# Kernel optimization log

Measured on AMD Instinct MI355X. Metric: run time of the kernel, lower is better.

Reference implementation:

```python
import jax, jax.numpy as jnp
import numpy as np

N_NODES = 50000


def gcn_conv(x, src, dst, norm, W, b, n_nodes):
    """One GCNConv layer: out = scatter_add(norm * (x @ W)[src] -> dst) + b.
    src/dst already include self loops; norm is the symmetric D^-1/2 A_hat D^-1/2 edge weight."""
    h = x @ W  # [N, C_out]
    msg = h[src] * norm[:, None]  # [E+N, C_out]
    out = jax.ops.segment_sum(msg, dst, num_segments=n_nodes)
    return out + b


def build_norm(edge_index, n_nodes):
    """Add self loops and compute symmetric GCN normalization (PyG GCNConv default)."""
    loop = jnp.arange(n_nodes, dtype=edge_index.dtype)
    src = jnp.concatenate([edge_index[0], loop])
    dst = jnp.concatenate([edge_index[1], loop])
    deg = jax.ops.segment_sum(jnp.ones_like(dst, dtype=jnp.float32), dst, num_segments=n_nodes)
    dinv = jnp.where(deg > 0, jax.lax.rsqrt(jnp.maximum(deg, 1.0)), 0.0)
    norm = dinv[src] * dinv[dst]
    return src, dst, norm


def setup_inputs() -> dict:
    key = jax.random.key(0)
    ks = jax.random.split(key, 8)
    in_c, h1, h2, out_c = 768, 256, 128, 2
    x = jax.random.normal(ks[0], (N_NODES, in_c), dtype=jnp.float32)
    edge_index = jax.random.randint(ks[1], (2, 800000), 0, N_NODES, dtype=jnp.int32)
    W1 = jax.random.normal(ks[2], (in_c, h1), dtype=jnp.float32) * 0.02
    b1 = jnp.zeros((h1,), dtype=jnp.float32)
    W2 = jax.random.normal(ks[3], (h1, h2), dtype=jnp.float32) * 0.02
    b2 = jnp.zeros((h2,), dtype=jnp.float32)
    W3 = jax.random.normal(ks[4], (h2, out_c), dtype=jnp.float32) * 0.02
    b3 = jnp.zeros((out_c,), dtype=jnp.float32)
    return {"x": x, "edge_index": edge_index, "W1": W1, "b1": b1,
            "W2": W2, "b2": b2, "W3": W3, "b3": b3}


def reference(x, edge_index, W1, b1, W2, b2, W3, b3):
    n = x.shape[0]
    src, dst, norm = build_norm(edge_index, n)
    # Dropout is identity in eval mode (training=False), so it is omitted.
    h = jax.nn.relu(gcn_conv(x, src, dst, norm, W1, b1, n))
    h = jax.nn.relu(gcn_conv(h, src, dst, norm, W2, b2, n))
    h = gcn_conv(h, src, dst, norm, W3, b3, n)
    return jax.nn.sigmoid(h)
```

## Files before the change

### kernel.cpp

```cpp
#include <hip/hip_runtime.h>
#include <math.h>

typedef short s16x8 __attribute__((ext_vector_type(8)));
typedef __bf16 b16x8 __attribute__((ext_vector_type(8)));
typedef float f32x4 __attribute__((ext_vector_type(4)));
typedef float f32x2 __attribute__((ext_vector_type(2)));
typedef unsigned int u32x4 __attribute__((ext_vector_type(4)));

__device__ inline short f2bf(float f) {
    unsigned u = __float_as_uint(f);
    unsigned r = u + 0x7FFFu + ((u >> 16) & 1u);
    return (short)(r >> 16);
}
__device__ inline float bf2f(unsigned short u) {
    return __uint_as_float(((unsigned)u) << 16);
}

#define GLDS16(g, l)                                                            \
    __builtin_amdgcn_global_load_lds(                                           \
        (const __attribute__((address_space(1))) void*)(g),                     \
        (__attribute__((address_space(3))) void*)(l), 16, 0, 0)


__device__ inline void make_wt_elem(const float* __restrict__ W, short* __restrict__ Wt,
                                    int K, int N, int idx) {
    int NB = N >> 7;
    int j = idx & 7;
    int l = (idx >> 3) & 63;
    int nt = (idx >> 9) & 7;
    int rest = idx >> 12;
    int b = rest % NB;
    int c = rest / NB;
    int k = c * 32 + (l >> 4) * 8 + j;
    int n = b * 128 + nt * 16 + (l & 15);
    Wt[idx] = f2bf(W[(size_t)k * N + n]);
}

__global__ void prep_kernel(const int* __restrict__ dst, int* __restrict__ cnt, int E,
                            const float* __restrict__ W1, short* __restrict__ Wt1,
                            const float* __restrict__ W2, short* __restrict__ Wt2,
                            int cb, int w1b) {
    int b = blockIdx.x;
    int tid = threadIdx.x;
    if (b < cb) {
        int e = b * 256 + tid;
        if (e < E) atomicAdd(&cnt[dst[e]], 1);
    } else if (b < cb + w1b) {
        int idx = (b - cb) * 256 + tid;
        make_wt_elem(W1, Wt1, 768, 256, idx);
    } else {
        int idx = (b - cb - w1b) * 256 + tid;
        make_wt_elem(W2, Wt2, 256, 128, idx);
    }
}


__global__ __launch_bounds__(1024) void blockscan_kernel(const int* __restrict__ cnt,
                                                         int* __restrict__ rp,
                                                         int* __restrict__ bsum, int n) {
    __shared__ int sdata[1024];
    int tid = threadIdx.x;
    int i = blockIdx.x * 1024 + tid;
    int v = (i < n) ? cnt[i] : 0;
    sdata[tid] = v;
    __syncthreads();
    for (int off = 1; off < 1024; off <<= 1) {
        int t = 0;
        if (tid >= off) t = sdata[tid - off];
        __syncthreads();
        sdata[tid] += t;
        __syncthreads();
    }
    if (i < n) rp[i] = sdata[tid] - v;
    if (tid == 1023) bsum[blockIdx.x] = sdata[1023];
}

__global__ void topscan_kernel(int* bsum, int nb) {
    int lane = threadIdx.x;
    int carry = 0;
    for (int base = 0; base < nb; base += 64) {
        int idx = base + lane;
        int orig = (idx < nb) ? bsum[idx] : 0;
        int v = orig;
        for (int off = 1; off < 64; off <<= 1) {
            int t = __shfl_up(v, off, 64);
            if (lane >= off) v += t;
        }
        if (idx < nb) bsum[idx] = carry + v - orig;
        carry += __shfl(v, 63, 64);
    }
}

__global__ __launch_bounds__(1024) void fixup_kernel(int* __restrict__ rp,
                                                     const int* __restrict__ bsum,
                                                     const int* __restrict__ cnt,
                                                     int* __restrict__ cursor,
                                                     float* __restrict__ dinv,
                                                     int n, int E) {
    int i = blockIdx.x * 1024 + threadIdx.x;
    if (i < n) {
        int r = rp[i] + bsum[blockIdx.x];
        rp[i] = r;
        cursor[i] = r;
        dinv[i] = rsqrtf((float)cnt[i] + 1.0f);
    }
    if (i == 0) rp[n] = E;
}

__global__ void fill_kernel(const int* __restrict__ src, const int* __restrict__ dst,
                            int* __restrict__ cursor, const float* __restrict__ dinv,
                            int* __restrict__ csrc, float* __restrict__ cw, int E) {
    int e = blockIdx.x * blockDim.x + threadIdx.x;
    if (e >= E) return;
    int d = dst[e];
    int s = src[e];
    int p = atomicAdd(&cursor[d], 1);
    csrc[p] = s;
    cw[p] = dinv[s] * dinv[d];
}


__global__ __launch_bounds__(256, 3) void gemm1_kernel(const float* __restrict__ x,
                                                       const short* __restrict__ Wt,
                                                       unsigned char* __restrict__ h8,
                                                       int M) {
    __shared__ float As[16 * 768];

    const int tid = threadIdx.x;
    const int lane = tid & 63;
    const int wave = tid >> 6;
    const int m0 = blockIdx.x * 16;

#pragma unroll
    for (int i = 0; i < 12; ++i) {
        int unit = wave * 12 + i;
        int row = unit / 3;
        int ch = unit - row * 3;
        GLDS16(x + (size_t)(m0 + row) * 768 + ch * 256 + lane * 4,
               &As[row * 768 + ch * 256]);
    }
    __syncthreads();

    const int q = lane >> 4;
    const int ml = lane & 15;
    const int b128 = wave >> 1;
    const int nt0 = (wave & 1) * 4;
    const s16x8* wt = (const s16x8*)Wt;
    const float4* af = (const float4*)As;

    f32x4 acc[4];
#pragma unroll
    for (int j = 0; j < 4; ++j) acc[j] = (f32x4){0.f, 0.f, 0.f, 0.f};

#pragma unroll 4
    for (int c = 0; c < 24; ++c) {
        int fi = ml * 192 + c * 8 + q * 2;
        float4 f0 = af[fi];
        float4 f1 = af[fi + 1];
        u32x4 pk;
        pk.x = (__float_as_uint(f0.x) >> 16) | (__float_as_uint(f0.y) & 0xFFFF0000u);
        pk.y = (__float_as_uint(f0.z) >> 16) | (__float_as_uint(f0.w) & 0xFFFF0000u);
        pk.z = (__float_as_uint(f1.x) >> 16) | (__float_as_uint(f1.y) & 0xFFFF0000u);
        pk.w = (__float_as_uint(f1.z) >> 16) | (__float_as_uint(f1.w) & 0xFFFF0000u);
        b16x8 areg = __builtin_bit_cast(b16x8, pk);

        b16x8 breg[4];
        size_t bb = (size_t)(c * 2 + b128) * 512 + nt0 * 64 + lane;
#pragma unroll
        for (int j = 0; j < 4; ++j)
            breg[j] = __builtin_bit_cast(b16x8, wt[bb + j * 64]);
#pragma unroll
        for (int j = 0; j < 4; ++j)
            acc[j] = __builtin_amdgcn_mfma_f32_16x16x32_bf16(areg, breg[j], acc[j], 0, 0, 0);
    }

    const int quad = lane >> 4;
    const int nl = lane & 15;
#pragma unroll
    for (int j = 0; j < 4; ++j) {
        int col = wave * 64 + j * 16 + nl;
#pragma unroll
        for (int r = 0; r < 4; ++r) {
            int row = m0 + quad * 4 + r;
            unsigned u = __builtin_amdgcn_cvt_pk_fp8_f32(acc[j][r], acc[j][r], 0, false);
            h8[(size_t)row * 256 + col] = (unsigned char)(u & 0xFF);
        }
    }
}


template<typename AT, int KC, int RT, int CW, int MINW>
__global__ __launch_bounds__(256, MINW) void gemm_panel_kernel(
        const AT* __restrict__ A, const short* __restrict__ Wt,
        unsigned short* __restrict__ Cb, int M) {
    constexpr int K = KC * 32;
    constexpr int O = KC * 4;
    constexpr int F = KC * RT / 4;
    constexpr int NCOLS = CW * 64;
    constexpr int NB = NCOLS >> 7;
    constexpr int MT = RT * CW / 4;

    __shared__ s16x8 As[KC * RT * 64];

    const int tid = threadIdx.x;
    const int m0 = blockIdx.x * (RT * 16);

    s16x8 v[F];
#pragma unroll
    for (int i = 0; i < F; ++i) {
        int idx = i * 256 + tid;
        int r = idx / O;
        int o = idx - r * O;
        int row = m0 + r;
        if (row >= M) row = M - 1;
        v[i] = *(const s16x8*)((const unsigned short*)A + (size_t)row * K + o * 8);
    }
#pragma unroll
    for (int i = 0; i < F; ++i) {
        int idx = i * 256 + tid;
        int r = idx / O;
        int o = idx - r * O;
        int c = o >> 2, q = o & 3;
        int slot = q * 16 + (((r & 15) + q + ((c & 3) << 2)) & 15);
        As[(c * RT + (r >> 4)) * 64 + slot] = v[i];
    }
    __syncthreads();

    const int lane = tid & 63;
    const int wave = tid >> 6;
    const int cw_i = wave % CW;
    const int rg = wave / CW;
    const int mtb = rg * MT;
    const int b128 = (cw_i * 64) >> 7;
    const int nt0 = (cw_i * 4) & 7;
    const int q = lane >> 4;
    const int rl = lane & 15;
    const s16x8* wt = (const s16x8*)Wt;

    f32x4 acc[MT][4];
#pragma unroll
    for (int i = 0; i < MT; ++i)
#pragma unroll
        for (int j = 0; j < 4; ++j)
            acc[i][j] = (f32x4){0.f, 0.f, 0.f, 0.f};

#pragma unroll 4
    for (int c = 0; c < KC; ++c) {
        int slot = q * 16 + ((rl + q + ((c & 3) << 2)) & 15);
        b16x8 areg[MT], breg[4];
#pragma unroll
        for (int i = 0; i < MT; ++i)
            areg[i] = __builtin_bit_cast(b16x8, As[(c * RT + mtb + i) * 64 + slot]);
        size_t bb = (size_t)(c * NB + b128) * 512 + nt0 * 64 + lane;
#pragma unroll
        for (int j = 0; j < 4; ++j)
            breg[j] = __builtin_bit_cast(b16x8, wt[bb + j * 64]);
#pragma unroll
        for (int i = 0; i < MT; ++i)
#pragma unroll
            for (int j = 0; j < 4; ++j)
                acc[i][j] = __builtin_amdgcn_mfma_f32_16x16x32_bf16(areg[i], breg[j], acc[i][j], 0, 0, 0);
    }

    const int quad = lane >> 4;
    const int nl = lane & 15;
#pragma unroll
    for (int i = 0; i < MT; ++i) {
        int rbase = m0 + (mtb + i) * 16 + quad * 4;
#pragma unroll
        for (int j = 0; j < 4; ++j) {
            int col = cw_i * 64 + j * 16 + nl;
#pragma unroll
            for (int rr = 0; rr < 4; ++rr) {
                int row = rbase + rr;
                if (row < M) Cb[(size_t)row * NCOLS + col] = (unsigned short)f2bf(acc[i][j][rr]);
            }
        }
    }
}


__global__ __launch_bounds__(256) void agg256_f8_kernel(const unsigned char* __restrict__ h8,
                                                        const int* __restrict__ rp,
                                                        const int* __restrict__ csrc,
                                                        const float* __restrict__ cw,
                                                        const float* __restrict__ dinv,
                                                        const float* __restrict__ bias,
                                                        unsigned short* __restrict__ out, int n) {
    int node = blockIdx.x * 4 + (threadIdx.x >> 6);
    int lane = threadIdx.x & 63;
    if (node >= n) return;
    const unsigned* hp = (const unsigned*)h8;
    float di = dinv[node];
    float ws = di * di;
    unsigned sv = hp[(size_t)node * 64 + lane];
    f32x2 slo = __builtin_amdgcn_cvt_pk_f32_fp8(sv, false);
    f32x2 shi = __builtin_amdgcn_cvt_pk_f32_fp8(sv, true);
    float a0 = ws * slo.x, a1 = ws * slo.y, a2 = ws * shi.x, a3 = ws * shi.y;
    int e = rp[node], e1 = rp[node + 1];
    for (; e + 1 < e1; e += 2) {
        int s0 = csrc[e], s1 = csrc[e + 1];
        float w0 = cw[e], w1 = cw[e + 1];
        unsigned v0 = hp[(size_t)s0 * 64 + lane];
        unsigned v1 = hp[(size_t)s1 * 64 + lane];
        f32x2 l0 = __builtin_amdgcn_cvt_pk_f32_fp8(v0, false);
        f32x2 h0 = __builtin_amdgcn_cvt_pk_f32_fp8(v0, true);
        f32x2 l1 = __builtin_amdgcn_cvt_pk_f32_fp8(v1, false);
        f32x2 h1 = __builtin_amdgcn_cvt_pk_f32_fp8(v1, true);
        a0 += w0 * l0.x + w1 * l1.x;
        a1 += w0 * l0.y + w1 * l1.y;
        a2 += w0 * h0.x + w1 * h1.x;
        a3 += w0 * h0.y + w1 * h1.y;
    }
    if (e < e1) {
        int s0 = csrc[e];
        float w0 = cw[e];
        unsigned v0 = hp[(size_t)s0 * 64 + lane];
        f32x2 l0 = __builtin_amdgcn_cvt_pk_f32_fp8(v0, false);
        f32x2 h0 = __builtin_amdgcn_cvt_pk_f32_fp8(v0, true);
        a0 += w0 * l0.x; a1 += w0 * l0.y; a2 += w0 * h0.x; a3 += w0 * h0.y;
    }
    float4 bv = *(const float4*)&bias[lane * 4];
    a0 = fmaxf(a0 + bv.x, 0.f); a1 = fmaxf(a1 + bv.y, 0.f);
    a2 = fmaxf(a2 + bv.z, 0.f); a3 = fmaxf(a3 + bv.w, 0.f);
    ushort4 ov;
    ov.x = (unsigned short)f2bf(a0); ov.y = (unsigned short)f2bf(a1);
    ov.z = (unsigned short)f2bf(a2); ov.w = (unsigned short)f2bf(a3);
    ((ushort4*)out)[(size_t)node * 64 + lane] = ov;
}

__global__ __launch_bounds__(256) void agg128_w3_kernel(const unsigned short* __restrict__ h,
                                                        const int* __restrict__ rp,
                                                        const int* __restrict__ csrc,
                                                        const float* __restrict__ cw,
                                                        const float* __restrict__ dinv,
                                                        const float* __restrict__ b2,
                                                        const float* __restrict__ W3,
                                                        float* __restrict__ z, int n) {
    int node = blockIdx.x * 4 + (threadIdx.x >> 6);
    int lane = threadIdx.x & 63;
    if (node >= n) return;
    const unsigned* hp = (const unsigned*)h;
    float di = dinv[node];
    float ws = di * di;
    unsigned sv = hp[(size_t)node * 64 + lane];
    float a0 = ws * __uint_as_float(sv << 16);
    float a1 = ws * __uint_as_float(sv & 0xFFFF0000u);
    int e = rp[node], e1 = rp[node + 1];
    for (; e + 1 < e1; e += 2) {
        int s0 = csrc[e], s1 = csrc[e + 1];
        float w0 = cw[e], w1 = cw[e + 1];
        unsigned v0 = hp[(size_t)s0 * 64 + lane];
        unsigned v1 = hp[(size_t)s1 * 64 + lane];
        a0 += w0 * __uint_as_float(v0 << 16) + w1 * __uint_as_float(v1 << 16);
        a1 += w0 * __uint_as_float(v0 & 0xFFFF0000u) + w1 * __uint_as_float(v1 & 0xFFFF0000u);
    }
    if (e < e1) {
        int s0 = csrc[e];
        float w0 = cw[e];
        unsigned v0 = hp[(size_t)s0 * 64 + lane];
        a0 += w0 * __uint_as_float(v0 << 16);
        a1 += w0 * __uint_as_float(v0 & 0xFFFF0000u);
    }
    float2 bv = *(const float2*)&b2[lane * 2];
    a0 = fmaxf(a0 + bv.x, 0.f);
    a1 = fmaxf(a1 + bv.y, 0.f);
    float4 wv = *(const float4*)&W3[lane * 4];
    float z0 = a0 * wv.x + a1 * wv.z;
    float z1 = a0 * wv.y + a1 * wv.w;
    for (int off = 32; off > 0; off >>= 1) {
        z0 += __shfl_down(z0, off, 64);
        z1 += __shfl_down(z1, off, 64);
    }
    if (lane == 0) {
        z[2 * (size_t)node] = z0;
        z[2 * (size_t)node + 1] = z1;
    }
}

__global__ void agg3_kernel(const float* __restrict__ z, const int* __restrict__ rp,
                            const int* __restrict__ csrc, const float* __restrict__ cw,
                            const float* __restrict__ dinv, const float* __restrict__ bias,
                            float* __restrict__ out, int n) {
    int node = blockIdx.x * blockDim.x + threadIdx.x;
    if (node >= n) return;
    float di = dinv[node];
    float a0 = di * di * z[2 * (size_t)node];
    float a1 = di * di * z[2 * (size_t)node + 1];
    int e1 = rp[node + 1];
    for (int e = rp[node]; e < e1; ++e) {
        int s = csrc[e];
        float w = cw[e];
        a0 += w * z[2 * (size_t)s];
        a1 += w * z[2 * (size_t)s + 1];
    }
    a0 += bias[0];
    a1 += bias[1];
    out[2 * (size_t)node]     = 1.f / (1.f + __expf(-a0));
    out[2 * (size_t)node + 1] = 1.f / (1.f + __expf(-a1));
}


extern "C" void kernel_launch(void* const* d_in, const int* in_sizes, int n_in,
                              void* d_out, int out_size, void* d_ws, size_t ws_size,
                              hipStream_t stream) {
    const float* x  = (const float*)d_in[0];
    const int*   ei = (const int*)d_in[1];
    const float* W1 = (const float*)d_in[2];
    const float* b1 = (const float*)d_in[3];
    const float* W2 = (const float*)d_in[4];
    const float* b2 = (const float*)d_in[5];
    const float* W3 = (const float*)d_in[6];
    const float* b3 = (const float*)d_in[7];
    float* out = (float*)d_out;

    const int E  = in_sizes[1] / 2;
    const int C1 = in_sizes[3];
    const int C2 = in_sizes[5];
    const int K1 = in_sizes[2] / C1;
    const int N  = in_sizes[0] / K1;

    const int* srcv = ei;
    const int* dstv = ei + E;

    char* p = (char*)d_ws;
    auto carve = [&](size_t bytes) {
        char* r = p;
        p += (bytes + 255) & ~(size_t)255;
        return r;
    };
    int*   cnt    = (int*)carve((size_t)N * 4);
    int*   rp     = (int*)carve((size_t)(N + 1) * 4);
    int*   cursor = (int*)carve((size_t)N * 4);
    float* dinv   = (float*)carve((size_t)N * 4);
    int*   bsum   = (int*)carve(1024 * 4);
    int*   csrc   = (int*)carve((size_t)E * 4);
    float* cw     = (float*)carve((size_t)E * 4);
    short* Wt1    = (short*)carve((size_t)K1 * C1 * 2);
    short* Wt2    = (short*)carve((size_t)C1 * C2 * 2);
    unsigned char* h8 = (unsigned char*)carve((size_t)N * C1);
    unsigned short* hB = (unsigned short*)carve((size_t)N * C1 * 2);
    unsigned short* h2 = (unsigned short*)carve((size_t)N * C2 * 2);
    float* zbuf   = (float*)carve((size_t)N * 2 * 4);

    const int nb = (N + 1023) / 1024;
    const int cb = (E + 255) / 256;
    const int w1b = (K1 * C1) / 256;
    const int w2b = (C1 * C2) / 256;

    hipMemsetAsync(cnt, 0, (size_t)N * 4, stream);
    prep_kernel<<<cb + w1b + w2b, 256, 0, stream>>>(dstv, cnt, E, W1, Wt1, W2, Wt2, cb, w1b);
    blockscan_kernel<<<nb, 1024, 0, stream>>>(cnt, rp, bsum, N);
    topscan_kernel<<<1, 64, 0, stream>>>(bsum, nb);
    fixup_kernel<<<nb, 1024, 0, stream>>>(rp, bsum, cnt, cursor, dinv, N, E);
    fill_kernel<<<(E + 255) / 256, 256, 0, stream>>>(srcv, dstv, cursor, dinv, csrc, cw, E);

    gemm1_kernel<<<N / 16, 256, 0, stream>>>(x, Wt1, h8, N);
    agg256_f8_kernel<<<(N + 3) / 4, 256, 0, stream>>>(h8, rp, csrc, cw, dinv, b1, hB, N);

    gemm_panel_kernel<unsigned short, 8, 4, 2, 4><<<(N + 63) / 64, 256, 0, stream>>>(hB, Wt2, h2, N);
    agg128_w3_kernel<<<(N + 3) / 4, 256, 0, stream>>>(h2, rp, csrc, cw, dinv, b2, W3, zbuf, N);

    agg3_kernel<<<(N + 255) / 256, 256, 0, stream>>>(zbuf, rp, csrc, cw, dinv, b3, out, N);
}
```

Measured before the change: 481.6 us.

## Tile gemm1 over 32 rows with register-staged bf16 LDS and swizzled layout

```diff
diff --git a/kernel.cpp b/kernel.cpp
--- a/kernel.cpp
+++ b/kernel.cpp
@@ -15,11 +15,6 @@
 __device__ inline float bf2f(unsigned short u) {
     return __uint_as_float(((unsigned)u) << 16);
 }
-
-#define GLDS16(g, l)                                                            \
-    __builtin_amdgcn_global_load_lds(                                           \
-        (const __attribute__((address_space(1))) void*)(g),                     \
-        (__attribute__((address_space(3))) void*)(l), 16, 0, 0)
 
 
 __device__ inline void make_wt_elem(const float* __restrict__ W, short* __restrict__ Wt,
@@ -124,66 +119,94 @@
                                                        const short* __restrict__ Wt,
                                                        unsigned char* __restrict__ h8,
                                                        int M) {
-    __shared__ float As[16 * 768];
+    constexpr int KC = 24;
+    constexpr int RT = 2;
+    constexpr int O = KC * 4;
+    constexpr int F = KC * RT * 64 / 256;
+
+    __shared__ s16x8 As[KC * RT * 64];
 
     const int tid = threadIdx.x;
-    const int lane = tid & 63;
-    const int wave = tid >> 6;
-    const int m0 = blockIdx.x * 16;
-
-#pragma unroll
-    for (int i = 0; i < 12; ++i) {
-        int unit = wave * 12 + i;
-        int row = unit / 3;
-        int ch = unit - row * 3;
-        GLDS16(x + (size_t)(m0 + row) * 768 + ch * 256 + lane * 4,
-               &As[row * 768 + ch * 256]);
-    }
-    __syncthreads();
-
-    const int q = lane >> 4;
-    const int ml = lane & 15;
-    const int b128 = wave >> 1;
-    const int nt0 = (wave & 1) * 4;
-    const s16x8* wt = (const s16x8*)Wt;
-    const float4* af = (const float4*)As;
-
-    f32x4 acc[4];
-#pragma unroll
-    for (int j = 0; j < 4; ++j) acc[j] = (f32x4){0.f, 0.f, 0.f, 0.f};
-
-#pragma unroll 4
-    for (int c = 0; c < 24; ++c) {
-        int fi = ml * 192 + c * 8 + q * 2;
-        float4 f0 = af[fi];
-        float4 f1 = af[fi + 1];
+    const int m0 = blockIdx.x * (RT * 16);
+
+    s16x8 v[F];
+#pragma unroll
+    for (int i = 0; i < F; ++i) {
+        int idx = i * 256 + tid;
+        int r = idx / O;
+        int o = idx - r * O;
+        int row = m0 + r;
+        if (row >= M) row = M - 1;
+        const float4* fp = (const float4*)(x + (size_t)row * 768 + o * 8);
+        float4 f0 = fp[0];
+        float4 f1 = fp[1];
         u32x4 pk;
         pk.x = (__float_as_uint(f0.x) >> 16) | (__float_as_uint(f0.y) & 0xFFFF0000u);
         pk.y = (__float_as_uint(f0.z) >> 16) | (__float_as_uint(f0.w) & 0xFFFF0000u);
         pk.z = (__float_as_uint(f1.x) >> 16) | (__float_as_uint(f1.y) & 0xFFFF0000u);
         pk.w = (__float_as_uint(f1.z) >> 16) | (__float_as_uint(f1.w) & 0xFFFF0000u);
-        b16x8 areg = __builtin_bit_cast(b16x8, pk);
-
-        b16x8 breg[4];
+        v[i] = __builtin_bit_cast(s16x8, pk);
+    }
+#pragma unroll
+    for (int i = 0; i < F; ++i) {
+        int idx = i * 256 + tid;
+        int r = idx / O;
+        int o = idx - r * O;
+        int c = o >> 2, q = o & 3;
+        int slot = q * 16 + (((r & 15) + q + ((c & 3) << 2)) & 15);
+        As[(c * RT + (r >> 4)) * 64 + slot] = v[i];
+    }
+    __syncthreads();
+
+    const int lane = tid & 63;
+    const int wave = tid >> 6;
+    const int b128 = wave >> 1;
+    const int nt0 = (wave & 1) * 4;
+    const int q = lane >> 4;
+    const int rl = lane & 15;
+    const s16x8* wt = (const s16x8*)Wt;
+
+    f32x4 acc[RT][4];
+#pragma unroll
+    for (int i = 0; i < RT; ++i)
+#pragma unroll
+        for (int j = 0; j < 4; ++j)
+            acc[i][j] = (f32x4){0.f, 0.f, 0.f, 0.f};
+
+#pragma unroll 4
+    for (int c = 0; c < KC; ++c) {
+        int slot = q * 16 + ((rl + q + ((c & 3) << 2)) & 15);
+        b16x8 areg[RT], breg[4];
+#pragma unroll
+        for (int i = 0; i < RT; ++i)
+            areg[i] = __builtin_bit_cast(b16x8, As[(c * RT + i) * 64 + slot]);
         size_t bb = (size_t)(c * 2 + b128) * 512 + nt0 * 64 + lane;
 #pragma unroll
         for (int j = 0; j < 4; ++j)
             breg[j] = __builtin_bit_cast(b16x8, wt[bb + j * 64]);
 #pragma unroll
-        for (int j = 0; j < 4; ++j)
-            acc[j] = __builtin_amdgcn_mfma_f32_16x16x32_bf16(areg, breg[j], acc[j], 0, 0, 0);
+        for (int i = 0; i < RT; ++i)
+#pragma unroll
+            for (int j = 0; j < 4; ++j)
+                acc[i][j] = __builtin_amdgcn_mfma_f32_16x16x32_bf16(areg[i], breg[j], acc[i][j], 0, 0, 0);
     }
 
     const int quad = lane >> 4;
     const int nl = lane & 15;
 #pragma unroll
-    for (int j = 0; j < 4; ++j) {
-        int col = wave * 64 + j * 16 + nl;
-#pragma unroll
-        for (int r = 0; r < 4; ++r) {
-            int row = m0 + quad * 4 + r;
-            unsigned u = __builtin_amdgcn_cvt_pk_fp8_f32(acc[j][r], acc[j][r], 0, false);
-            h8[(size_t)row * 256 + col] = (unsigned char)(u & 0xFF);
+    for (int i = 0; i < RT; ++i) {
+        int rbase = m0 + i * 16 + quad * 4;
+#pragma unroll
+        for (int j = 0; j < 4; ++j) {
+            int col = wave * 64 + j * 16 + nl;
+#pragma unroll
+            for (int r = 0; r < 4; ++r) {
+                int row = rbase + r;
+                if (row < M) {
+                    unsigned u = __builtin_amdgcn_cvt_pk_fp8_f32(acc[i][j][r], acc[i][j][r], 0, false);
+                    h8[(size_t)row * 256 + col] = (unsigned char)(u & 0xFF);
+                }
+            }
         }
     }
 }
@@ -455,7 +478,7 @@
     fixup_kernel<<<nb, 1024, 0, stream>>>(rp, bsum, cnt, cursor, dinv, N, E);
     fill_kernel<<<(E + 255) / 256, 256, 0, stream>>>(srcv, dstv, cursor, dinv, csrc, cw, E);
 
-    gemm1_kernel<<<N / 16, 256, 0, stream>>>(x, Wt1, h8, N);
+    gemm1_kernel<<<(N + 31) / 32, 256, 0, stream>>>(x, Wt1, h8, N);
     agg256_f8_kernel<<<(N + 3) / 4, 256, 0, stream>>>(h8, rp, csrc, cw, dinv, b1, hB, N);
 
     gemm_panel_kernel<unsigned short, 8, 4, 2, 4><<<(N + 63) / 64, 256, 0, stream>>>(hB, Wt2, h2, N);
```

Result: no change. 488.4 us (+1.4%).
